# Optimization experiments

Measured on AMD Instinct MI355X. Metric: run time of the kernel, lower is better.

Reference implementation:

```python
import jax, jax.numpy as jnp
import numpy as np
from jax import lax

DIM = 256
SEQ = 1024
BATCH = 4
EPS = 1e-6
P_TANH_SCALE = 10.0


def setup_inputs() -> dict:
    key = jax.random.key(0)
    ks = jax.random.split(key, 12)
    d, n, b = DIM, SEQ, BATCH
    half = d // 2
    x = jax.random.normal(ks[0], (b, n, d), jnp.float32)
    # RoPE frequencies (standard llama-style), complex freqs_cis split into cos/sin
    inv_freq = 1.0 / (10000.0 ** (np.arange(half, dtype=np.float64) * 2.0 / d))
    ang = np.outer(np.arange(n, dtype=np.float64), inv_freq)  # (n, d/2)
    freqs_cis_cos = jnp.asarray(np.cos(ang), jnp.float32)
    freqs_cis_sin = jnp.asarray(np.sin(ang), jnp.float32)
    s = 1.0 / np.sqrt(d)
    Wqkv = jax.random.normal(ks[1], (3 * d, d), jnp.float32) * s
    qconv_w = jax.random.normal(ks[2], (d, 4), jnp.float32) * 0.3
    qconv_b = jax.random.normal(ks[3], (d,), jnp.float32) * 0.02
    kconv_w = jax.random.normal(ks[4], (d, 4), jnp.float32) * 0.3
    kconv_b = jax.random.normal(ks[5], (d,), jnp.float32) * 0.02
    vconv_w = jax.random.normal(ks[6], (d, 4), jnp.float32) * 0.3
    vconv_b = jax.random.normal(ks[7], (d,), jnp.float32) * 0.02
    Wparam = jax.random.normal(ks[8], (2, d), jnp.float32) * s
    bparam = jnp.zeros((2,), jnp.float32)
    W0 = jnp.eye(d, dtype=jnp.float32)  # nn.init.eye_
    Wgate = jax.random.normal(ks[9], (d, d), jnp.float32) * s
    Wout = jax.random.normal(ks[10], (d, d), jnp.float32) * s
    return dict(x=x, freqs_cis_cos=freqs_cis_cos, freqs_cis_sin=freqs_cis_sin,
                Wqkv=Wqkv, qconv_w=qconv_w, qconv_b=qconv_b,
                kconv_w=kconv_w, kconv_b=kconv_b, vconv_w=vconv_w, vconv_b=vconv_b,
                Wparam=Wparam, bparam=bparam, W0=W0, Wgate=Wgate, Wout=Wout)


def _causal_dwconv(x, w, bias):
    # x: (b,n,d); w: (d,4); torch Conv1d(k=4, pad=3, groups=d) truncated to [:n]
    # y[t] = sum_j w[:,j] * x[t-3+j]  (zero left-pad)
    b, n, d = x.shape
    xp = jnp.pad(x, ((0, 0), (3, 0), (0, 0)))
    y = sum(xp[:, j:j + n, :] * w[None, None, :, j] for j in range(4))
    return y + bias[None, None, :]


def _rope(x, cos, sin):
    # x: (b,n,d); pairs (x[...,2i], x[...,2i+1]) rotated by freqs_cis
    xr, xi = x[..., 0::2], x[..., 1::2]
    c, s = cos[None], sin[None]
    outr = xr * c - xi * s
    outi = xr * s + xi * c
    return jnp.stack((outr, outi), axis=-1).reshape(x.shape)


def _l2norm(x):
    nrm = jnp.linalg.norm(x, axis=-1, keepdims=True)
    return x / jnp.maximum(nrm, 1e-12)


def _forward(x, cos, sin, Wqkv, qw, qb, kw, kb, vw, vb, Wparam, bparam, W0, Wgate, Wout):
    b, n, d = x.shape
    qkv = x @ Wqkv.T
    q, k, v = jnp.split(qkv, 3, axis=-1)
    q = _causal_dwconv(q, qw, qb)
    k = _causal_dwconv(k, kw, kb)
    v = _causal_dwconv(v, vw, vb)
    q = _l2norm(_rope(q, cos, sin))
    k = _l2norm(_rope(k, cos, sin))
    params = x @ Wparam.T + bparam  # (b,n,2)
    eta = jax.nn.sigmoid(params[..., 0])    # (b,n)
    alpha = jax.nn.sigmoid(params[..., 1])  # (b,n)

    def step(carry, inp):
        A, W = carry                      # (b,d,d)
        qt, kt, vt, et, at = inp          # (b,d)x3, (b,)x2
        pred = jnp.einsum('bd,bde->be', kt, W)
        diff = pred - vt
        grad_pred = 3.0 * jnp.tanh(P_TANH_SCALE * diff) * (diff * diff)  # p == 3
        grad_W = kt[:, :, None] * grad_pred[:, None, :]
        A = at[:, None, None] * A - et[:, None, None] * grad_W
        a4 = jnp.square(jnp.square(A))  # q == 4
        denom = jnp.sqrt(a4.sum(axis=(-2, -1), keepdims=True)) + EPS
        W = A / denom
        yt = jnp.einsum('bd,bde->be', qt, W)
        return (A, W), yt

    A0 = jnp.zeros((b, d, d), x.dtype)
    W_init = jnp.broadcast_to(W0, (b, d, d)).astype(x.dtype)
    xs = (q.transpose(1, 0, 2), k.transpose(1, 0, 2), v.transpose(1, 0, 2),
          eta.T, alpha.T)
    _, yT = lax.scan(jax.checkpoint(step), (A0, W_init), xs)
    y = yT.transpose(1, 0, 2)  # (b,n,d)
    return (y @ Wout.T) * jax.nn.sigmoid(x @ Wgate.T)


def reference(x, freqs_cis_cos, freqs_cis_sin, Wqkv, qconv_w, qconv_b,
              kconv_w, kconv_b, vconv_w, vconv_b, Wparam, bparam, W0, Wgate, Wout):
    return _forward(x, freqs_cis_cos, freqs_cis_sin, Wqkv, qconv_w, qconv_b,
                    kconv_w, kconv_b, vconv_w, vconv_b, Wparam, bparam, W0, Wgate, Wout)
```

## Files before the change

kernel.cpp:

```cpp
#include <hip/hip_runtime.h>

#define DIMD 256
#define SEQT 1024
#define NB   4

typedef float v2f __attribute__((ext_vector_type(2)));
#define FMA2(a,b,c) __builtin_elementwise_fma((a),(b),(c))

__device__ __forceinline__ float sigmoidf_(float x){ return 1.0f/(1.0f+expf(-x)); }

template<int EPI>
__global__ __launch_bounds__(256) void gemm_bt(const float* __restrict__ A,
    const float* __restrict__ Bm, float* __restrict__ C, int N,
    const float* __restrict__ gpre)
{
  __shared__ float sA[64][68];
  __shared__ float sB[64][68];
  const int nb = N >> 6;
  const int bm = blockIdx.x / nb, bn = blockIdx.x - bm*nb;
  const int m0 = bm << 6, n0 = bn << 6;
  const int tid = threadIdx.x;
  const int tr = tid >> 4, tc = tid & 15;
  float acc[4][4];
  #pragma unroll
  for (int i=0;i<4;i++)
    #pragma unroll
    for (int j=0;j<4;j++) acc[i][j]=0.f;

  for (int kc=0;kc<4;kc++){
    __syncthreads();
    for (int i=tid;i<1024;i+=256){
      int r = i >> 4, q4 = i & 15;
      *(float4*)&sA[r][q4*4] = ((const float4*)(A  + (m0+r)*256 + kc*64))[q4];
      *(float4*)&sB[r][q4*4] = ((const float4*)(Bm + (n0+r)*256 + kc*64))[q4];
    }
    __syncthreads();
    #pragma unroll
    for (int kq=0;kq<16;kq++){
      float4 av[4], bv[4];
      #pragma unroll
      for (int i=0;i<4;i++) av[i] = *(const float4*)&sA[tr+16*i][kq*4];
      #pragma unroll
      for (int j=0;j<4;j++) bv[j] = *(const float4*)&sB[tc+16*j][kq*4];
      #pragma unroll
      for (int i=0;i<4;i++)
        #pragma unroll
        for (int j=0;j<4;j++)
          acc[i][j] = fmaf(av[i].x,bv[j].x, fmaf(av[i].y,bv[j].y,
                      fmaf(av[i].z,bv[j].z, fmaf(av[i].w,bv[j].w, acc[i][j]))));
    }
  }
  #pragma unroll
  for (int i=0;i<4;i++){
    #pragma unroll
    for (int j=0;j<4;j++){
      int m = m0 + tr + 16*i, n = n0 + tc + 16*j;
      float val = acc[i][j];
      if (EPI==1) val *= sigmoidf_(gpre[m*N+n]);
      C[m*N+n] = val;
    }
  }
}

__global__ __launch_bounds__(256) void prep_kernel(
    const float* __restrict__ qkvr, const float* __restrict__ x,
    const float* __restrict__ cosT, const float* __restrict__ sinT,
    const float* __restrict__ qw, const float* __restrict__ qbias,
    const float* __restrict__ kw, const float* __restrict__ kbias,
    const float* __restrict__ vw, const float* __restrict__ vbias,
    const float* __restrict__ Wparam, const float* __restrict__ bparam,
    float* __restrict__ qo, float* __restrict__ ko, float* __restrict__ vo,
    float* __restrict__ eo, float* __restrict__ ao)
{
  const int bt = blockIdx.x;
  const int t = bt & 1023;
  const int d = threadIdx.x;

  float4 wq = ((const float4*)qw)[d];
  float4 wk = ((const float4*)kw)[d];
  float4 wv = ((const float4*)vw)[d];
  const float wqj[4] = {wq.x,wq.y,wq.z,wq.w};
  const float wkj[4] = {wk.x,wk.y,wk.z,wk.w};
  const float wvj[4] = {wv.x,wv.y,wv.z,wv.w};
  float qa = qbias[d], ka = kbias[d], va = vbias[d];
  #pragma unroll
  for (int j=0;j<4;j++){
    int tt = t - 3 + j;
    if (tt >= 0) {
      const float* row = qkvr + (size_t)(bt - 3 + j) * 768;
      qa = fmaf(row[d],      wqj[j], qa);
      ka = fmaf(row[256+d],  wkj[j], ka);
      va = fmaf(row[512+d],  wvj[j], va);
    }
  }
  vo[bt*256 + d] = va;

  __shared__ float sq[256], sk[256];
  __shared__ float red[4][4];
  sq[d] = qa; sk[d] = ka;
  __syncthreads();
  const int i = d >> 1;
  const float c = cosT[t*128 + i], s = sinT[t*128 + i];
  float qr, krp;
  if ((d & 1) == 0) { qr = sq[d]*c - sq[d+1]*s;  krp = sk[d]*c - sk[d+1]*s; }
  else              { qr = sq[d-1]*s + sq[d]*c;  krp = sk[d-1]*s + sk[d]*c; }

  const float xd = x[bt*256 + d];
  float r0 = qr*qr, r1 = krp*krp, r2 = xd*Wparam[d], r3 = xd*Wparam[256+d];
  #pragma unroll
  for (int m=1;m<64;m<<=1){
    r0 += __shfl_xor(r0, m, 64);
    r1 += __shfl_xor(r1, m, 64);
    r2 += __shfl_xor(r2, m, 64);
    r3 += __shfl_xor(r3, m, 64);
  }
  const int w = d >> 6;
  if ((d & 63) == 0){ red[w][0]=r0; red[w][1]=r1; red[w][2]=r2; red[w][3]=r3; }
  __syncthreads();
  float qss = red[0][0]+red[1][0]+red[2][0]+red[3][0];
  float kss = red[0][1]+red[1][1]+red[2][1]+red[3][1];
  qo[bt*256+d] = qr  / fmaxf(sqrtf(qss), 1e-12f);
  ko[bt*256+d] = krp / fmaxf(sqrtf(kss), 1e-12f);
  if (d == 0){
    float p0 = red[0][2]+red[1][2]+red[2][2]+red[3][2] + bparam[0];
    float p1 = red[0][3]+red[1][3]+red[2][3]+red[3][3] + bparam[1];
    eo[bt] = 1.f/(1.f+expf(-p0));
    ao[bt] = 1.f/(1.f+expf(-p1));
  }
}

__global__ __launch_bounds__(1024, 4) void scan_kernel(
    const float* __restrict__ qn, const float* __restrict__ kn,
    const float* __restrict__ vn, const float* __restrict__ eta,
    const float* __restrict__ alpha, const float* __restrict__ W0,
    float* __restrict__ y)
{
  const int b = blockIdx.x;
  const int tid = threadIdx.x;
  const int rg = tid >> 8;
  const int c  = tid & 255;
  const int r0 = rg << 6;

  __shared__ float s_k[2][256], s_q[2][256], s_v[2][256];
  __shared__ float s_ea[2][2];
  __shared__ float part[4][256], part2[4][256];
  __shared__ float s_s4[16];

  v2f A2[32];
  #pragma unroll
  for (int j=0;j<32;j++) A2[j] = (v2f)(0.f);

  const float* kb = kn + b*SEQT*DIMD;
  const float* qb = qn + b*SEQT*DIMD;
  const float* vb = vn + b*SEQT*DIMD;
  const float* eb = eta   + b*SEQT;
  const float* ab = alpha + b*SEQT;
  float* yb = y + b*SEQT*DIMD;

  if (tid < 64)        ((float4*)s_k[0])[tid]      = ((const float4*)kb)[tid];
  else if (tid < 128)  ((float4*)s_q[0])[tid-64]   = ((const float4*)qb)[tid-64];
  else if (tid < 192)  ((float4*)s_v[0])[tid-128]  = ((const float4*)vb)[tid-128];
  if (tid == 192) { s_ea[0][0] = eb[0]; s_ea[0][1] = ab[0]; }
  __syncthreads();

  float inv_prev = 1.0f;

  for (int t=0; t<SEQT; ++t) {
    const int cur = t & 1, nxt = cur ^ 1;

    float4 pf = make_float4(0.f,0.f,0.f,0.f);
    float pe = 0.f, pa = 0.f;
    if (t+1 < SEQT) {
      if (tid < 64)       pf = ((const float4*)(kb + (t+1)*DIMD))[tid];
      else if (tid < 128) pf = ((const float4*)(qb + (t+1)*DIMD))[tid-64];
      else if (tid < 192) pf = ((const float4*)(vb + (t+1)*DIMD))[tid-128];
      if (tid == 192) { pe = eb[t+1]; pa = ab[t+1]; }
    }

    float d0;
    if (t == 0) {
      const float* w0p = W0 + (size_t)r0*DIMD + c;
      float acc = 0.f;
      #pragma unroll
      for (int j=0;j<64;j++)
        acc = fmaf(s_k[0][r0+j], w0p[(size_t)j*DIMD], acc);
      d0 = acc;
    } else {
      const float4* kp = (const float4*)(s_k[cur] + r0);
      v2f acc0 = (v2f)(0.f), acc1 = (v2f)(0.f);
      #pragma unroll
      for (int jq=0;jq<16;jq++){
        float4 kv = kp[jq];
        v2f klo = {kv.x, kv.y}, khi = {kv.z, kv.w};
        acc0 = FMA2(klo, A2[2*jq],   acc0);
        acc1 = FMA2(khi, A2[2*jq+1], acc1);
      }
      d0 = ((acc0.x + acc0.y) + (acc1.x + acc1.y)) * inv_prev;
    }
    part[rg][c] = d0;
    __syncthreads();

    float pr = part[0][c]+part[1][c]+part[2][c]+part[3][c];
    const float et = s_ea[cur][0], al = s_ea[cur][1];
    float df = pr - s_v[cur][c];
    float e  = __expf(20.f*df);
    float th = 1.f - 2.f*__builtin_amdgcn_rcpf(e + 1.f);
    float t0 = et * 3.f * th * (df*df);

    const v2f alv = {al, al};
    const v2f nt0 = {-t0, -t0};
    v2f s4a = (v2f)(0.f), s4b = (v2f)(0.f);
    v2f u2a = (v2f)(0.f), u2b = (v2f)(0.f);
    {
      const float4* kp = (const float4*)(s_k[cur] + r0);
      const float4* qp = (const float4*)(s_q[cur] + r0);
      #pragma unroll
      for (int jq=0;jq<16;jq++){
        float4 kv = kp[jq], qv = qp[jq];
        v2f klo = {kv.x, kv.y}, khi = {kv.z, kv.w};
        v2f qlo = {qv.x, qv.y}, qhi = {qv.z, qv.w};
        v2f a, a2;
        a = FMA2(alv, A2[2*jq],   nt0*klo); A2[2*jq]   = a;
        a2 = a*a; s4a = FMA2(a2, a2, s4a);  u2a = FMA2(qlo, a, u2a);
        a = FMA2(alv, A2[2*jq+1], nt0*khi); A2[2*jq+1] = a;
        a2 = a*a; s4b = FMA2(a2, a2, s4b);  u2b = FMA2(qhi, a, u2b);
      }
    }
    part2[rg][c] = (u2a.x + u2a.y) + (u2b.x + u2b.y);
    float s4 = (s4a.x + s4a.y) + (s4b.x + s4b.y);

    #pragma unroll
    for (int m=1;m<64;m<<=1) s4 += __shfl_xor(s4, m, 64);
    if ((tid & 63) == 0) s_s4[tid>>6] = s4;

    if (t+1 < SEQT) {
      if (tid < 64)       ((float4*)s_k[nxt])[tid]     = pf;
      else if (tid < 128) ((float4*)s_q[nxt])[tid-64]  = pf;
      else if (tid < 192) ((float4*)s_v[nxt])[tid-128] = pf;
      if (tid == 192) { s_ea[nxt][0]=pe; s_ea[nxt][1]=pa; }
    }
    __syncthreads();

    float4 sa = ((const float4*)s_s4)[0], sb = ((const float4*)s_s4)[1];
    float4 sc = ((const float4*)s_s4)[2], sd = ((const float4*)s_s4)[3];
    float s4t = ((sa.x+sa.y)+(sa.z+sa.w)) + ((sb.x+sb.y)+(sb.z+sb.w))
              + ((sc.x+sc.y)+(sc.z+sc.w)) + ((sd.x+sd.y)+(sd.z+sd.w));
    float w   = sqrtf(s4t) + 1e-6f;
    float r   = __builtin_amdgcn_rcpf(w);
    r = r * (2.f - w*r);
    if (rg == 0)
      yb[t*DIMD + c] = (part2[0][c]+part2[1][c]+part2[2][c]+part2[3][c]) * r;
    inv_prev = r;
  }
}

extern "C" void kernel_launch(void* const* d_in, const int* in_sizes, int n_in,
                              void* d_out, int out_size, void* d_ws, size_t ws_size,
                              hipStream_t stream)
{
  const float* x     = (const float*)d_in[0];
  const float* cosT  = (const float*)d_in[1];
  const float* sinT  = (const float*)d_in[2];
  const float* Wqkv  = (const float*)d_in[3];
  const float* qw    = (const float*)d_in[4];
  const float* qb    = (const float*)d_in[5];
  const float* kw    = (const float*)d_in[6];
  const float* kb    = (const float*)d_in[7];
  const float* vw    = (const float*)d_in[8];
  const float* vb    = (const float*)d_in[9];
  const float* Wparam= (const float*)d_in[10];
  const float* bparam= (const float*)d_in[11];
  const float* W0    = (const float*)d_in[12];
  const float* Wgate = (const float*)d_in[13];
  const float* Wout  = (const float*)d_in[14];
  float* out = (float*)d_out;

  float* ws    = (float*)d_ws;
  float* qkvr  = ws;
  float* qn    = qkvr + 4*1024*768;
  float* kn    = qn   + 4*1024*256;
  float* vn    = kn   + 4*1024*256;
  float* eta   = vn   + 4*1024*256;
  float* alpha = eta  + 4096;
  float* yv    = qkvr;
  float* tmpg  = qkvr + 1048576;

  gemm_bt<0><<<dim3(64*12), 256, 0, stream>>>(x, Wqkv, qkvr, 768, nullptr);
  prep_kernel<<<dim3(4096), 256, 0, stream>>>(qkvr, x, cosT, sinT,
      qw, qb, kw, kb, vw, vb, Wparam, bparam, qn, kn, vn, eta, alpha);
  scan_kernel<<<dim3(NB), 1024, 0, stream>>>(qn, kn, vn, eta, alpha, W0, yv);
  gemm_bt<0><<<dim3(64*4), 256, 0, stream>>>(x, Wgate, tmpg, 256, nullptr);
  gemm_bt<1><<<dim3(64*4), 256, 0, stream>>>(yv, Wout, out, 256, tmpg);
}
```

Measured before the change: 3.091 ms.

## Restructure scan kernel to one barrier per step with lane-interleaved row groups

Rows of the per-batch scan are now split across adjacent lanes (rg = tid&3) instead of across 256-thread groups. Partial dot products can then be reduced with wave shuffles rather than shared-memory part arrays, which removes one of the two __syncthreads per timestep. The normalisation and output store are deferred to the next step through a double-buffered s4 array. k/q/v staging becomes triple-buffered with a two-step-ahead prefetch, and k/q rows are padded to avoid bank conflicts. In exchange the design relies on subtler buffer-reuse ordering and adds shuffles and some extra register pressure.

```diff
diff --git a/kernel.cpp b/kernel.cpp
--- a/kernel.cpp
+++ b/kernel.cpp
@@ -3,6 +3,7 @@
 #define DIMD 256
 #define SEQT 1024
 #define NB   4
+#define KSTRIDE 272
 
 typedef float v2f __attribute__((ext_vector_type(2)));
 #define FMA2(a,b,c) __builtin_elementwise_fma((a),(b),(c))
@@ -137,14 +138,14 @@
 {
   const int b = blockIdx.x;
   const int tid = threadIdx.x;
-  const int rg = tid >> 8;
-  const int c  = tid & 255;
+  const int rg = tid & 3;
+  const int c  = tid >> 2;
   const int r0 = rg << 6;
-
-  __shared__ float s_k[2][256], s_q[2][256], s_v[2][256];
-  __shared__ float s_ea[2][2];
-  __shared__ float part[4][256], part2[4][256];
-  __shared__ float s_s4[16];
+  const int koff = 68 * rg;
+
+  __shared__ float s_k[3][KSTRIDE], s_q[3][KSTRIDE], s_v[3][256];
+  __shared__ float s_ea[3][2];
+  __shared__ float s_s4[2][16];
 
   v2f A2[32];
   #pragma unroll
@@ -157,36 +158,51 @@
   const float* ab = alpha + b*SEQT;
   float* yb = y + b*SEQT*DIMD;
 
-  if (tid < 64)        ((float4*)s_k[0])[tid]      = ((const float4*)kb)[tid];
-  else if (tid < 128)  ((float4*)s_q[0])[tid-64]   = ((const float4*)qb)[tid-64];
-  else if (tid < 192)  ((float4*)s_v[0])[tid-128]  = ((const float4*)vb)[tid-128];
+  if (tid < 64) {
+    float4 v0 = ((const float4*)kb)[tid];
+    *(float4*)&s_k[0][4*tid + (tid>>4)*4] = v0;
+  } else if (tid < 128) {
+    int i = tid-64;
+    float4 v0 = ((const float4*)qb)[i];
+    *(float4*)&s_q[0][4*i + (i>>4)*4] = v0;
+  } else if (tid < 192) {
+    ((float4*)s_v[0])[tid-128] = ((const float4*)vb)[tid-128];
+  }
   if (tid == 192) { s_ea[0][0] = eb[0]; s_ea[0][1] = ab[0]; }
+
+  float4 pf = make_float4(0.f,0.f,0.f,0.f);
+  float pe = 0.f, pa = 0.f;
+  if (tid < 64)       pf = ((const float4*)(kb + DIMD))[tid];
+  else if (tid < 128) pf = ((const float4*)(qb + DIMD))[tid-64];
+  else if (tid < 192) pf = ((const float4*)(vb + DIMD))[tid-128];
+  if (tid == 192) { pe = eb[1]; pa = ab[1]; }
   __syncthreads();
 
   float inv_prev = 1.0f;
+  float u_prev = 0.f;
+  int cur = 0;
 
   for (int t=0; t<SEQT; ++t) {
-    const int cur = t & 1, nxt = cur ^ 1;
-
-    float4 pf = make_float4(0.f,0.f,0.f,0.f);
-    float pe = 0.f, pa = 0.f;
+    const int nxt = (cur==2) ? 0 : cur+1;
+
     if (t+1 < SEQT) {
-      if (tid < 64)       pf = ((const float4*)(kb + (t+1)*DIMD))[tid];
-      else if (tid < 128) pf = ((const float4*)(qb + (t+1)*DIMD))[tid-64];
-      else if (tid < 192) pf = ((const float4*)(vb + (t+1)*DIMD))[tid-128];
-      if (tid == 192) { pe = eb[t+1]; pa = ab[t+1]; }
-    }
-
-    float d0;
+      if (tid < 64)       *(float4*)&s_k[nxt][4*tid + (tid>>4)*4] = pf;
+      else if (tid < 128){ int i = tid-64; *(float4*)&s_q[nxt][4*i + (i>>4)*4] = pf; }
+      else if (tid < 192) ((float4*)s_v[nxt])[tid-128] = pf;
+      if (tid == 192) { s_ea[nxt][0]=pe; s_ea[nxt][1]=pa; }
+    }
+
+    float pred_raw;
     if (t == 0) {
       const float* w0p = W0 + (size_t)r0*DIMD + c;
+      const float* kq = s_k[0] + koff;
       float acc = 0.f;
       #pragma unroll
       for (int j=0;j<64;j++)
-        acc = fmaf(s_k[0][r0+j], w0p[(size_t)j*DIMD], acc);
-      d0 = acc;
+        acc = fmaf(kq[j], w0p[(size_t)j*DIMD], acc);
+      pred_raw = acc;
     } else {
-      const float4* kp = (const float4*)(s_k[cur] + r0);
+      const float4* kp = (const float4*)(s_k[cur] + koff);
       v2f acc0 = (v2f)(0.f), acc1 = (v2f)(0.f);
       #pragma unroll
       for (int jq=0;jq<16;jq++){
@@ -195,14 +211,36 @@
         acc0 = FMA2(klo, A2[2*jq],   acc0);
         acc1 = FMA2(khi, A2[2*jq+1], acc1);
       }
-      d0 = ((acc0.x + acc0.y) + (acc1.x + acc1.y)) * inv_prev;
-    }
-    part[rg][c] = d0;
+      pred_raw = (acc0.x + acc0.y) + (acc1.x + acc1.y);
+    }
+    pred_raw += __shfl_xor(pred_raw, 1, 64);
+    pred_raw += __shfl_xor(pred_raw, 2, 64);
+
     __syncthreads();
 
-    float pr = part[0][c]+part[1][c]+part[2][c]+part[3][c];
+    if (t+2 < SEQT) {
+      if (tid < 64)       pf = ((const float4*)(kb + (t+2)*DIMD))[tid];
+      else if (tid < 128) pf = ((const float4*)(qb + (t+2)*DIMD))[tid-64];
+      else if (tid < 192) pf = ((const float4*)(vb + (t+2)*DIMD))[tid-128];
+      if (tid == 192) { pe = eb[t+2]; pa = ab[t+2]; }
+    }
+
+    if (t > 0) {
+      const float* sp = s_s4[(t-1)&1];
+      float4 sa = ((const float4*)sp)[0], sb4 = ((const float4*)sp)[1];
+      float4 sc4= ((const float4*)sp)[2], sd4 = ((const float4*)sp)[3];
+      float s4t = ((sa.x+sa.y)+(sa.z+sa.w)) + ((sb4.x+sb4.y)+(sb4.z+sb4.w))
+                + ((sc4.x+sc4.y)+(sc4.z+sc4.w)) + ((sd4.x+sd4.y)+(sd4.z+sd4.w));
+      float w = sqrtf(s4t) + 1e-6f;
+      float r = __builtin_amdgcn_rcpf(w);
+      r = r * (2.f - w*r);
+      inv_prev = r;
+      if (rg == 0) yb[(t-1)*DIMD + c] = u_prev * r;
+    }
+
+    float pred = pred_raw * inv_prev;
     const float et = s_ea[cur][0], al = s_ea[cur][1];
-    float df = pr - s_v[cur][c];
+    float df = pred - s_v[cur][c];
     float e  = __expf(20.f*df);
     float th = 1.f - 2.f*__builtin_amdgcn_rcpf(e + 1.f);
     float t0 = et * 3.f * th * (df*df);
@@ -212,8 +250,8 @@
     v2f s4a = (v2f)(0.f), s4b = (v2f)(0.f);
     v2f u2a = (v2f)(0.f), u2b = (v2f)(0.f);
     {
-      const float4* kp = (const float4*)(s_k[cur] + r0);
-      const float4* qp = (const float4*)(s_q[cur] + r0);
+      const float4* kp = (const float4*)(s_k[cur] + koff);
+      const float4* qp = (const float4*)(s_q[cur] + koff);
       #pragma unroll
       for (int jq=0;jq<16;jq++){
         float4 kv = kp[jq], qv = qp[jq];
@@ -226,31 +264,30 @@
         a2 = a*a; s4b = FMA2(a2, a2, s4b);  u2b = FMA2(qhi, a, u2b);
       }
     }
-    part2[rg][c] = (u2a.x + u2a.y) + (u2b.x + u2b.y);
+    float u = (u2a.x + u2a.y) + (u2b.x + u2b.y);
+    u += __shfl_xor(u, 1, 64);
+    u += __shfl_xor(u, 2, 64);
+    u_prev = u;
+
     float s4 = (s4a.x + s4a.y) + (s4b.x + s4b.y);
-
     #pragma unroll
     for (int m=1;m<64;m<<=1) s4 += __shfl_xor(s4, m, 64);
-    if ((tid & 63) == 0) s_s4[tid>>6] = s4;
-
-    if (t+1 < SEQT) {
-      if (tid < 64)       ((float4*)s_k[nxt])[tid]     = pf;
-      else if (tid < 128) ((float4*)s_q[nxt])[tid-64]  = pf;
-      else if (tid < 192) ((float4*)s_v[nxt])[tid-128] = pf;
-      if (tid == 192) { s_ea[nxt][0]=pe; s_ea[nxt][1]=pa; }
-    }
-    __syncthreads();
-
-    float4 sa = ((const float4*)s_s4)[0], sb = ((const float4*)s_s4)[1];
-    float4 sc = ((const float4*)s_s4)[2], sd = ((const float4*)s_s4)[3];
-    float s4t = ((sa.x+sa.y)+(sa.z+sa.w)) + ((sb.x+sb.y)+(sb.z+sb.w))
-              + ((sc.x+sc.y)+(sc.z+sc.w)) + ((sd.x+sd.y)+(sd.z+sd.w));
-    float w   = sqrtf(s4t) + 1e-6f;
-    float r   = __builtin_amdgcn_rcpf(w);
+    if ((tid & 63) == 0) s_s4[t&1][tid>>6] = s4;
+
+    cur = nxt;
+  }
+
+  __syncthreads();
+  {
+    const float* sp = s_s4[1];
+    float4 sa = ((const float4*)sp)[0], sb4 = ((const float4*)sp)[1];
+    float4 sc4= ((const float4*)sp)[2], sd4 = ((const float4*)sp)[3];
+    float s4t = ((sa.x+sa.y)+(sa.z+sa.w)) + ((sb4.x+sb4.y)+(sb4.z+sb4.w))
+              + ((sc4.x+sc4.y)+(sc4.z+sc4.w)) + ((sd4.x+sd4.y)+(sd4.z+sd4.w));
+    float w = sqrtf(s4t) + 1e-6f;
+    float r = __builtin_amdgcn_rcpf(w);
     r = r * (2.f - w*r);
-    if (rg == 0)
-      yb[t*DIMD + c] = (part2[0][c]+part2[1][c]+part2[2][c]+part2[3][c]) * r;
-    inv_prev = r;
+    if (rg == 0) yb[1023*DIMD + c] = u_prev * r;
   }
 }
 
```

Measured after the change: 3.051 ms. About the same (-1.3%).
